# Performance work log

Measured on AMD Instinct MI355X. Metric: run time of the kernel, lower is better.

Reference implementation:

```python
import jax, jax.numpy as jnp
import numpy as np

C = 256
CK = C // 8  # key/query channels

def setup_inputs() -> dict:
    key = jax.random.key(0)
    ks = jax.random.split(key, 8)
    x = jax.random.normal(ks[0], (4, C, 64, 64), dtype=jnp.float32)
    # 1x1 conv weights stored as (out_ch, in_ch); bias (out_ch,)
    Wb = jax.random.normal(ks[1], (CK, C), dtype=jnp.float32) * (1.0 / np.sqrt(C))
    bb = jnp.zeros((CK,), dtype=jnp.float32)
    Wc = jax.random.normal(ks[2], (CK, C), dtype=jnp.float32) * (1.0 / np.sqrt(C))
    bc = jnp.zeros((CK,), dtype=jnp.float32)
    Wd = jax.random.normal(ks[3], (C, C), dtype=jnp.float32) * (1.0 / np.sqrt(C))
    bd = jnp.zeros((C,), dtype=jnp.float32)
    gamma = jnp.zeros((1,), dtype=jnp.float32)
    return {"x": x, "Wb": Wb, "bb": bb, "Wc": Wc, "bc": bc, "Wd": Wd, "bd": bd, "gamma": gamma}

def reference(x, Wb, bb, Wc, bc, Wd, bd, gamma):
    B, Cc, H, W = x.shape
    N = H * W
    xf = x.reshape(B, Cc, N)                                  # (B, C, N)
    # 1x1 convs == per-pixel linear projections
    b = jnp.einsum('kc,bcn->bnk', Wb, xf) + bb                # (B, N, CK) queries
    c = jnp.einsum('kc,bcn->bkn', Wc, xf) + bc[None, :, None] # (B, CK, N) keys
    d = jnp.einsum('oc,bcn->bon', Wd, xf) + bd[None, :, None] # (B, C, N) values
    attn = jax.nn.softmax(jnp.einsum('bnk,bkm->bnm', b, c), axis=-1)  # (B, N, N)
    out = jnp.einsum('bcm,bnm->bcn', d, attn).reshape(B, Cc, H, W)
    return gamma[0] * out + x
```

## Files before the change

### kernel.cpp

```cpp
#include <hip/hip_runtime.h>
#include <math.h>

#define B_  4
#define C_  256
#define N_  4096
#define NT  (N_ / 64)

typedef __attribute__((ext_vector_type(8)))  short v8s;
typedef __attribute__((ext_vector_type(4)))  float v4f;
typedef __attribute__((ext_vector_type(16))) float v16f;

__device__ inline unsigned short f2bf(float f) {
    unsigned u = __builtin_bit_cast(unsigned, f);
    unsigned r = (u + 0x7fffu + ((u >> 16) & 1u)) >> 16;
    return (unsigned short)r;
}
__device__ inline unsigned cvtpk(float lo, float hi) {
    unsigned r;
    asm("v_cvt_pk_bf16_f32 %0, %1, %2" : "=v"(r) : "v"(lo), "v"(hi));
    return r;
}
__device__ inline void swap32(unsigned &a, unsigned &b) {
    asm volatile("v_permlane32_swap_b32 %0, %1" : "+v"(a), "+v"(b));
}
__device__ inline void gl_lds16(const void* g, void* l) {
    __builtin_amdgcn_global_load_lds(
        (const __attribute__((address_space(1))) unsigned*)g,
        (__attribute__((address_space(3))) unsigned*)l, 16, 0, 0);
}

__global__ __launch_bounds__(256) void wcvt_kernel(
    const float* __restrict__ Wb, const float* __restrict__ Wc,
    const float* __restrict__ Wd, unsigned short* __restrict__ Wcat)
{
    int i = (blockIdx.x * 256 + threadIdx.x) * 4;
    int row = i >> 8, col = i & 255;
    const float* src;
    if (row < 256)      src = Wd + row * 256 + col;
    else if (row < 288) src = Wb + (row - 256) * 256 + col;
    else                src = Wc + (row - 288) * 256 + col;
    float4 v = *(const float4*)src;
    uint2 p;
    p.x = cvtpk(v.x, v.y);
    p.y = cvtpk(v.z, v.w);
    *(uint2*)(Wcat + i) = p;
}

#define PXS 264
__global__ __launch_bounds__(256, 2) void proj_mfma(
    const float* __restrict__ x, const unsigned short* __restrict__ Wcat,
    const float* __restrict__ bb, const float* __restrict__ bc,
    const float* __restrict__ bd,
    unsigned short* __restrict__ Q, unsigned short* __restrict__ K,
    unsigned short* __restrict__ V)
{
    __shared__ unsigned short Xs[32][PXS];
    const int t = threadIdx.x;
    const int w = t >> 6, l = t & 63, l16 = l & 15, lg = l >> 4;
    const int n0 = blockIdx.x * 32, b = blockIdx.y;

    {
        const int n = t & 31, g = t >> 5;
        const int c0 = g * 32;
        const float* xp = x + (size_t)b * C_ * N_ + n0 + n;
#pragma unroll
        for (int hf = 0; hf < 2; hf++) {
            unsigned pk[4];
#pragma unroll
            for (int j = 0; j < 4; j++) {
                int c = c0 + hf * 16 + 2 * j;
                pk[j] = cvtpk(xp[(size_t)c * N_], xp[(size_t)(c + 1) * N_]);
            }
            *(uint4*)&Xs[n][c0 + hf * 16] = make_uint4(pk[0], pk[1], pk[2], pk[3]);
        }
    }
    __syncthreads();

#pragma unroll 1
    for (int si = 0; si < 5; si++) {
        const int sub = w * 5 + si;

        v8s aw[8];
#pragma unroll
        for (int kk = 0; kk < 8; kk++)
            aw[kk] = *(const v8s*)(Wcat + (size_t)(sub * 16 + l16) * 256 + kk * 32 + lg * 8);

        v4f acc[2];
#pragma unroll
        for (int ns = 0; ns < 2; ns++) { v4f z = {0.f,0.f,0.f,0.f}; acc[ns] = z; }

#pragma unroll
        for (int kk = 0; kk < 8; kk++)
#pragma unroll
            for (int ns = 0; ns < 2; ns++) {
                v8s bx = *(const v8s*)&Xs[ns * 16 + l16][kk * 32 + lg * 8];
                acc[ns] = __builtin_amdgcn_mfma_f32_16x16x32_bf16(aw[kk], bx, acc[ns], 0, 0, 0);
            }

        if (sub < 16) {
            float bi[4];
#pragma unroll
            for (int r = 0; r < 4; r++) bi[r] = bd[sub * 16 + lg * 4 + r];
#pragma unroll
            for (int ns = 0; ns < 2; ns++) {
                const int n = n0 + ns * 16 + l16;
#pragma unroll
                for (int r = 0; r < 4; r++) {
                    int c = sub * 16 + lg * 4 + r;
                    V[((size_t)b * C_ + c) * N_ + n] = f2bf(acc[ns][r] + bi[r]);
                }
            }
        } else {
            const int qk = sub - 16;
            const bool isQ = (qk < 2);
            const int o0l = (qk & 1) * 16;
            const float* bias = isQ ? bb : bc;
            unsigned short* dst = isQ ? Q : K;
            float bi[4];
#pragma unroll
            for (int r = 0; r < 4; r++) bi[r] = bias[o0l + lg * 4 + r];
#pragma unroll
            for (int ns = 0; ns < 2; ns++) {
                const int n = n0 + ns * 16 + l16;
                uint2 pk;
                pk.x = cvtpk(acc[ns][0] + bi[0], acc[ns][1] + bi[1]);
                pk.y = cvtpk(acc[ns][2] + bi[2], acc[ns][3] + bi[3]);
                *(uint2*)(dst + ((size_t)b * N_ + n) * 32 + o0l + lg * 4) = pk;
            }
        }
    }
}

__global__ __launch_bounds__(256, 2) void attn_mfma(
    const unsigned short* __restrict__ Qg, const unsigned short* __restrict__ Kg,
    const unsigned short* __restrict__ Vg, const float* __restrict__ x,
    const float* __restrict__ gamma, float* __restrict__ out)
{
    __shared__ unsigned short Vs[2][64][64];

    const int t = threadIdx.x, l = t & 63, cl = l & 31, h = l >> 5;
    const int qs = t >> 6;
    const int i = blockIdx.x;
    const int xcd = i & 7, b = xcd >> 1, ch_hi = xcd & 1;
    const int rdec = i >> 3, ch = ch_hi * 2 + (rdec & 1), qb = rdec >> 1;
    const int q0 = qb * 128;
    const int q = q0 + qs * 32 + cl;

    const unsigned short* qp = Qg + ((size_t)b * N_ + q) * 32 + h * 8;
    const v8s bQ0 = *(const v8s*)(qp);
    const v8s bQ1 = *(const v8s*)(qp + 16);

    const unsigned short* kp = Kg + ((size_t)b * N_ + cl) * 32 + h * 8;
    const unsigned short* Vb = Vg + ((size_t)b * C_ + ch * 64) * N_;
    const int vrow = t >> 3;
    const int vslot = (t & 7) ^ (vrow & 7);
    const unsigned short* vsrc0 = Vb + (size_t)vrow * N_ + vslot * 8;
    const unsigned short* vsrc1 = Vb + (size_t)(32 + vrow) * N_ + vslot * 8;
    char* const ldsw = (char*)&Vs[0][0][0] + (t >> 6) * 1024;

    v16f acc0, acc1;
#pragma unroll
    for (int r = 0; r < 16; r++) { acc0[r] = 0.f; acc1[r] = 0.f; }
    float l_lane = 0.f;

    gl_lds16(vsrc0, ldsw);
    gl_lds16(vsrc1, ldsw + 4096);
    v8s kc0a = *(const v8s*)(kp);
    v8s kc0b = *(const v8s*)(kp + 16);
    v8s kc1a = *(const v8s*)(kp + 1024);
    v8s kc1b = *(const v8s*)(kp + 1024 + 16);
    __syncthreads();

    const int sx0 = ((0 * 2 + h) ^ (l & 7)) << 4;
    const int sx1 = ((1 * 2 + h) ^ (l & 7)) << 4;
    const int sx2 = ((2 * 2 + h) ^ (l & 7)) << 4;
    const int sx3 = ((3 * 2 + h) ^ (l & 7)) << 4;

#pragma unroll 1
    for (int it = 0; it < NT; it++) {
        const int buf = it & 1;
        v8s kn0a, kn0b, kn1a, kn1b;
        if (it + 1 < NT) {
            const int m1 = (it + 1) * 64;
            gl_lds16(vsrc0 + m1, ldsw + (buf ^ 1) * 8192);
            gl_lds16(vsrc1 + m1, ldsw + (buf ^ 1) * 8192 + 4096);
            const unsigned short* kpm = kp + (size_t)m1 * 32;
            kn0a = *(const v8s*)(kpm);
            kn0b = *(const v8s*)(kpm + 16);
            kn1a = *(const v8s*)(kpm + 1024);
            kn1b = *(const v8s*)(kpm + 1024 + 16);
        }

        v16f st0, st1;
#pragma unroll
        for (int r = 0; r < 16; r++) { st0[r] = 0.f; st1[r] = 0.f; }
        st0 = __builtin_amdgcn_mfma_f32_32x32x16_bf16(kc0a, bQ0, st0, 0, 0, 0);
        st0 = __builtin_amdgcn_mfma_f32_32x32x16_bf16(kc0b, bQ1, st0, 0, 0, 0);
        st1 = __builtin_amdgcn_mfma_f32_32x32x16_bf16(kc1a, bQ0, st1, 0, 0, 0);
        st1 = __builtin_amdgcn_mfma_f32_32x32x16_bf16(kc1b, bQ1, st1, 0, 0, 0);

        float ps = 0.f;
#pragma unroll
        for (int r = 0; r < 16; r++) { st0[r] = __expf(st0[r]); ps += st0[r]; }
#pragma unroll
        for (int r = 0; r < 16; r++) { st1[r] = __expf(st1[r]); ps += st1[r]; }
        l_lane += ps;

        unsigned pbw[4][4];
#pragma unroll
        for (int ms = 0; ms < 2; ms++) {
#pragma unroll
            for (int kl = 0; kl < 2; kl++) {
#pragma unroll
                for (int wl = 0; wl < 2; wl++) {
                    float e0, e1, f0, f1;
                    if (ms == 0) {
                        e0 = st0[(2*kl+0)*4 + 2*wl]; e1 = st0[(2*kl+0)*4 + 2*wl + 1];
                        f0 = st0[(2*kl+1)*4 + 2*wl]; f1 = st0[(2*kl+1)*4 + 2*wl + 1];
                    } else {
                        e0 = st1[(2*kl+0)*4 + 2*wl]; e1 = st1[(2*kl+0)*4 + 2*wl + 1];
                        f0 = st1[(2*kl+1)*4 + 2*wl]; f1 = st1[(2*kl+1)*4 + 2*wl + 1];
                    }
                    unsigned a = cvtpk(e0, e1);
                    unsigned c = cvtpk(f0, f1);
                    swap32(a, c);
                    pbw[ms * 2 + kl][wl]     = a;
                    pbw[ms * 2 + kl][2 + wl] = c;
                }
            }
        }

        const char* vbse = (const char*)&Vs[buf][0][0];
        {
            union { unsigned u[4]; v8s v; } pb;
#pragma unroll
            for (int ks2 = 0; ks2 < 4; ks2++) {
                pb.u[0] = pbw[ks2][0]; pb.u[1] = pbw[ks2][1];
                pb.u[2] = pbw[ks2][2]; pb.u[3] = pbw[ks2][3];
                const int sx = (ks2 == 0) ? sx0 : (ks2 == 1) ? sx1 : (ks2 == 2) ? sx2 : sx3;
                v8s a0 = *(const v8s*)(vbse + (cl << 7) + sx);
                v8s a1 = *(const v8s*)(vbse + ((32 + cl) << 7) + sx);
                acc0 = __builtin_amdgcn_mfma_f32_32x32x16_bf16(a0, pb.v, acc0, 0, 0, 0);
                acc1 = __builtin_amdgcn_mfma_f32_32x32x16_bf16(a1, pb.v, acc1, 0, 0, 0);
            }
        }

        __syncthreads();
        kc0a = kn0a; kc0b = kn0b; kc1a = kn1a; kc1b = kn1b;
    }

    float l_tot = l_lane + __shfl_xor(l_lane, 32);
    const float il = 1.0f / l_tot;
    const float gm = gamma[0];
#pragma unroll
    for (int cs = 0; cs < 2; cs++) {
#pragma unroll
        for (int r = 0; r < 16; r++) {
            int c = ch * 64 + cs * 32 + (r & 3) + 8 * (r >> 2) + 4 * h;
            size_t idx = ((size_t)b * C_ + c) * N_ + q;
            float a = (cs == 0) ? acc0[r] : acc1[r];
            out[idx] = gm * (a * il) + x[idx];
        }
    }
}

extern "C" void kernel_launch(void* const* d_in, const int* in_sizes, int n_in,
                              void* d_out, int out_size, void* d_ws, size_t ws_size,
                              hipStream_t stream)
{
    const float* x  = (const float*)d_in[0];
    const float* Wb = (const float*)d_in[1];
    const float* bb = (const float*)d_in[2];
    const float* Wc = (const float*)d_in[3];
    const float* bc = (const float*)d_in[4];
    const float* Wd = (const float*)d_in[5];
    const float* bd = (const float*)d_in[6];
    const float* gm = (const float*)d_in[7];
    float* out = (float*)d_out;

    unsigned short* Qw = (unsigned short*)d_ws;
    unsigned short* Kw = Qw + (size_t)B_ * N_ * 32;
    unsigned short* Vw = Kw + (size_t)B_ * N_ * 32;
    unsigned short* Wcat = Vw + (size_t)B_ * C_ * N_;

    wcvt_kernel<<<dim3(80), 256, 0, stream>>>(Wb, Wc, Wd, Wcat);
    proj_mfma<<<dim3(N_ / 32, B_), 256, 0, stream>>>(x, Wcat, bb, bc, bd, Qw, Kw, Vw);
    attn_mfma<<<dim3(512), 256, 0, stream>>>(Qw, Kw, Vw, x, gm, out);
}
```

Before: 163.8 us.

## Software-pipeline PV MFMA one tile behind QK, fold log2e into Q, vectorize x load

The attention loop now defers the P·V MFMAs for tile it-1 into iteration it, so they issue between the QK MFMAs and the exp of the current tile. This lets the matrix unit overlap with the softmax VALU work. The V LDS ring grows from 2 to 4 buffers so the deferred tile stays valid while later tiles load. Q is prescaled by log2(e) in the projection so the loop can use exp2f instead of __expf. The projection's x load is changed to float4 reads with scalar bf16 stores into LDS. Costs are more LDS per block, a larger live register set from the carried P fragments, and possible bank conflicts from the scalar LDS stores.

```diff
diff --git a/kernel.cpp b/kernel.cpp
--- a/kernel.cpp
+++ b/kernel.cpp
@@ -5,6 +5,7 @@
 #define C_  256
 #define N_  4096
 #define NT  (N_ / 64)
+#define LOG2E 1.44269504088896f
 
 typedef __attribute__((ext_vector_type(8)))  short v8s;
 typedef __attribute__((ext_vector_type(4)))  float v4f;
@@ -60,18 +61,16 @@
     const int n0 = blockIdx.x * 32, b = blockIdx.y;
 
     {
-        const int n = t & 31, g = t >> 5;
-        const int c0 = g * 32;
-        const float* xp = x + (size_t)b * C_ * N_ + n0 + n;
-#pragma unroll
-        for (int hf = 0; hf < 2; hf++) {
-            unsigned pk[4];
-#pragma unroll
-            for (int j = 0; j < 4; j++) {
-                int c = c0 + hf * 16 + 2 * j;
-                pk[j] = cvtpk(xp[(size_t)c * N_], xp[(size_t)(c + 1) * N_]);
-            }
-            *(uint4*)&Xs[n][c0 + hf * 16] = make_uint4(pk[0], pk[1], pk[2], pk[3]);
+        const int n4 = (t & 7) * 4, cb = t >> 3;
+        const float* xp = x + (size_t)b * C_ * N_ + n0 + n4;
+#pragma unroll
+        for (int r = 0; r < 8; r++) {
+            const int c = cb + r * 32;
+            float4 v = *(const float4*)(xp + (size_t)c * N_);
+            Xs[n4 + 0][c] = f2bf(v.x);
+            Xs[n4 + 1][c] = f2bf(v.y);
+            Xs[n4 + 2][c] = f2bf(v.z);
+            Xs[n4 + 3][c] = f2bf(v.w);
         }
     }
     __syncthreads();
@@ -79,7 +78,6 @@
 #pragma unroll 1
     for (int si = 0; si < 5; si++) {
         const int sub = w * 5 + si;
-
         v8s aw[8];
 #pragma unroll
         for (int kk = 0; kk < 8; kk++)
@@ -88,7 +86,6 @@
         v4f acc[2];
 #pragma unroll
         for (int ns = 0; ns < 2; ns++) { v4f z = {0.f,0.f,0.f,0.f}; acc[ns] = z; }
-
 #pragma unroll
         for (int kk = 0; kk < 8; kk++)
 #pragma unroll
@@ -116,6 +113,7 @@
             const int o0l = (qk & 1) * 16;
             const float* bias = isQ ? bb : bc;
             unsigned short* dst = isQ ? Q : K;
+            const float scl = isQ ? LOG2E : 1.0f;
             float bi[4];
 #pragma unroll
             for (int r = 0; r < 4; r++) bi[r] = bias[o0l + lg * 4 + r];
@@ -123,8 +121,8 @@
             for (int ns = 0; ns < 2; ns++) {
                 const int n = n0 + ns * 16 + l16;
                 uint2 pk;
-                pk.x = cvtpk(acc[ns][0] + bi[0], acc[ns][1] + bi[1]);
-                pk.y = cvtpk(acc[ns][2] + bi[2], acc[ns][3] + bi[3]);
+                pk.x = cvtpk((acc[ns][0] + bi[0]) * scl, (acc[ns][1] + bi[1]) * scl);
+                pk.y = cvtpk((acc[ns][2] + bi[2]) * scl, (acc[ns][3] + bi[3]) * scl);
                 *(uint2*)(dst + ((size_t)b * N_ + n) * 32 + o0l + lg * 4) = pk;
             }
         }
@@ -136,7 +134,7 @@
     const unsigned short* __restrict__ Vg, const float* __restrict__ x,
     const float* __restrict__ gamma, float* __restrict__ out)
 {
-    __shared__ unsigned short Vs[2][64][64];
+    __shared__ unsigned short Vs[4][64][64];
 
     const int t = threadIdx.x, l = t & 63, cl = l & 31, h = l >> 5;
     const int qs = t >> 6;
@@ -156,34 +154,36 @@
     const int vslot = (t & 7) ^ (vrow & 7);
     const unsigned short* vsrc0 = Vb + (size_t)vrow * N_ + vslot * 8;
     const unsigned short* vsrc1 = Vb + (size_t)(32 + vrow) * N_ + vslot * 8;
-    char* const ldsw = (char*)&Vs[0][0][0] + (t >> 6) * 1024;
+    const int wofs = (t >> 6) * 1024;
 
     v16f acc0, acc1;
 #pragma unroll
     for (int r = 0; r < 16; r++) { acc0[r] = 0.f; acc1[r] = 0.f; }
     float l_lane = 0.f;
 
-    gl_lds16(vsrc0, ldsw);
-    gl_lds16(vsrc1, ldsw + 4096);
+    gl_lds16(vsrc0, (char*)&Vs[0][0][0] + wofs);
+    gl_lds16(vsrc1, (char*)&Vs[0][0][0] + wofs + 4096);
     v8s kc0a = *(const v8s*)(kp);
     v8s kc0b = *(const v8s*)(kp + 16);
     v8s kc1a = *(const v8s*)(kp + 1024);
     v8s kc1b = *(const v8s*)(kp + 1024 + 16);
     __syncthreads();
 
-    const int sx0 = ((0 * 2 + h) ^ (l & 7)) << 4;
-    const int sx1 = ((1 * 2 + h) ^ (l & 7)) << 4;
-    const int sx2 = ((2 * 2 + h) ^ (l & 7)) << 4;
-    const int sx3 = ((3 * 2 + h) ^ (l & 7)) << 4;
+    const int sx0 = ((0 + h) ^ (l & 7)) << 4;
+    const int sx1 = ((2 + h) ^ (l & 7)) << 4;
+    const int sx2 = ((4 + h) ^ (l & 7)) << 4;
+    const int sx3 = ((6 + h) ^ (l & 7)) << 4;
+
+    v8s pbP0, pbP1, pbP2, pbP3;
 
 #pragma unroll 1
     for (int it = 0; it < NT; it++) {
-        const int buf = it & 1;
         v8s kn0a, kn0b, kn1a, kn1b;
         if (it + 1 < NT) {
             const int m1 = (it + 1) * 64;
-            gl_lds16(vsrc0 + m1, ldsw + (buf ^ 1) * 8192);
-            gl_lds16(vsrc1 + m1, ldsw + (buf ^ 1) * 8192 + 4096);
+            char* vd = (char*)&Vs[(it + 1) & 3][0][0] + wofs;
+            gl_lds16(vsrc0 + m1, vd);
+            gl_lds16(vsrc1 + m1, vd + 4096);
             const unsigned short* kpm = kp + (size_t)m1 * 32;
             kn0a = *(const v8s*)(kpm);
             kn0b = *(const v8s*)(kpm + 16);
@@ -199,11 +199,31 @@
         st1 = __builtin_amdgcn_mfma_f32_32x32x16_bf16(kc1a, bQ0, st1, 0, 0, 0);
         st1 = __builtin_amdgcn_mfma_f32_32x32x16_bf16(kc1b, bQ1, st1, 0, 0, 0);
 
+        if (it > 0) {
+            const char* vbse = (const char*)&Vs[(it - 1) & 3][0][0];
+            v8s a00 = *(const v8s*)(vbse + (cl << 7) + sx0);
+            v8s a10 = *(const v8s*)(vbse + ((32 + cl) << 7) + sx0);
+            v8s a01 = *(const v8s*)(vbse + (cl << 7) + sx1);
+            v8s a11 = *(const v8s*)(vbse + ((32 + cl) << 7) + sx1);
+            v8s a02 = *(const v8s*)(vbse + (cl << 7) + sx2);
+            v8s a12 = *(const v8s*)(vbse + ((32 + cl) << 7) + sx2);
+            v8s a03 = *(const v8s*)(vbse + (cl << 7) + sx3);
+            v8s a13 = *(const v8s*)(vbse + ((32 + cl) << 7) + sx3);
+            acc0 = __builtin_amdgcn_mfma_f32_32x32x16_bf16(a00, pbP0, acc0, 0, 0, 0);
+            acc1 = __builtin_amdgcn_mfma_f32_32x32x16_bf16(a10, pbP0, acc1, 0, 0, 0);
+            acc0 = __builtin_amdgcn_mfma_f32_32x32x16_bf16(a01, pbP1, acc0, 0, 0, 0);
+            acc1 = __builtin_amdgcn_mfma_f32_32x32x16_bf16(a11, pbP1, acc1, 0, 0, 0);
+            acc0 = __builtin_amdgcn_mfma_f32_32x32x16_bf16(a02, pbP2, acc0, 0, 0, 0);
+            acc1 = __builtin_amdgcn_mfma_f32_32x32x16_bf16(a12, pbP2, acc1, 0, 0, 0);
+            acc0 = __builtin_amdgcn_mfma_f32_32x32x16_bf16(a03, pbP3, acc0, 0, 0, 0);
+            acc1 = __builtin_amdgcn_mfma_f32_32x32x16_bf16(a13, pbP3, acc1, 0, 0, 0);
+        }
+
         float ps = 0.f;
 #pragma unroll
-        for (int r = 0; r < 16; r++) { st0[r] = __expf(st0[r]); ps += st0[r]; }
-#pragma unroll
-        for (int r = 0; r < 16; r++) { st1[r] = __expf(st1[r]); ps += st1[r]; }
+        for (int r = 0; r < 16; r++) { st0[r] = exp2f(st0[r]); ps += st0[r]; }
+#pragma unroll
+        for (int r = 0; r < 16; r++) { st1[r] = exp2f(st1[r]); ps += st1[r]; }
         l_lane += ps;
 
         unsigned pbw[4][4];
@@ -229,24 +249,36 @@
                 }
             }
         }
-
-        const char* vbse = (const char*)&Vs[buf][0][0];
         {
-            union { unsigned u[4]; v8s v; } pb;
-#pragma unroll
-            for (int ks2 = 0; ks2 < 4; ks2++) {
-                pb.u[0] = pbw[ks2][0]; pb.u[1] = pbw[ks2][1];
-                pb.u[2] = pbw[ks2][2]; pb.u[3] = pbw[ks2][3];
-                const int sx = (ks2 == 0) ? sx0 : (ks2 == 1) ? sx1 : (ks2 == 2) ? sx2 : sx3;
-                v8s a0 = *(const v8s*)(vbse + (cl << 7) + sx);
-                v8s a1 = *(const v8s*)(vbse + ((32 + cl) << 7) + sx);
-                acc0 = __builtin_amdgcn_mfma_f32_32x32x16_bf16(a0, pb.v, acc0, 0, 0, 0);
-                acc1 = __builtin_amdgcn_mfma_f32_32x32x16_bf16(a1, pb.v, acc1, 0, 0, 0);
-            }
+            union { unsigned u[4]; v8s v; } f;
+            f.u[0]=pbw[0][0]; f.u[1]=pbw[0][1]; f.u[2]=pbw[0][2]; f.u[3]=pbw[0][3]; pbP0=f.v;
+            f.u[0]=pbw[1][0]; f.u[1]=pbw[1][1]; f.u[2]=pbw[1][2]; f.u[3]=pbw[1][3]; pbP1=f.v;
+            f.u[0]=pbw[2][0]; f.u[1]=pbw[2][1]; f.u[2]=pbw[2][2]; f.u[3]=pbw[2][3]; pbP2=f.v;
+            f.u[0]=pbw[3][0]; f.u[1]=pbw[3][1]; f.u[2]=pbw[3][2]; f.u[3]=pbw[3][3]; pbP3=f.v;
         }
 
         __syncthreads();
         kc0a = kn0a; kc0b = kn0b; kc1a = kn1a; kc1b = kn1b;
+    }
+
+    {
+        const char* vbse = (const char*)&Vs[(NT - 1) & 3][0][0];
+        v8s a00 = *(const v8s*)(vbse + (cl << 7) + sx0);
+        v8s a10 = *(const v8s*)(vbse + ((32 + cl) << 7) + sx0);
+        v8s a01 = *(const v8s*)(vbse + (cl << 7) + sx1);
+        v8s a11 = *(const v8s*)(vbse + ((32 + cl) << 7) + sx1);
+        v8s a02 = *(const v8s*)(vbse + (cl << 7) + sx2);
+        v8s a12 = *(const v8s*)(vbse + ((32 + cl) << 7) + sx2);
+        v8s a03 = *(const v8s*)(vbse + (cl << 7) + sx3);
+        v8s a13 = *(const v8s*)(vbse + ((32 + cl) << 7) + sx3);
+        acc0 = __builtin_amdgcn_mfma_f32_32x32x16_bf16(a00, pbP0, acc0, 0, 0, 0);
+        acc1 = __builtin_amdgcn_mfma_f32_32x32x16_bf16(a10, pbP0, acc1, 0, 0, 0);
+        acc0 = __builtin_amdgcn_mfma_f32_32x32x16_bf16(a01, pbP1, acc0, 0, 0, 0);
+        acc1 = __builtin_amdgcn_mfma_f32_32x32x16_bf16(a11, pbP1, acc1, 0, 0, 0);
+        acc0 = __builtin_amdgcn_mfma_f32_32x32x16_bf16(a02, pbP2, acc0, 0, 0, 0);
+        acc1 = __builtin_amdgcn_mfma_f32_32x32x16_bf16(a12, pbP2, acc1, 0, 0, 0);
+        acc0 = __builtin_amdgcn_mfma_f32_32x32x16_bf16(a03, pbP3, acc0, 0, 0, 0);
+        acc1 = __builtin_amdgcn_mfma_f32_32x32x16_bf16(a13, pbP3, acc1, 0, 0, 0);
     }
 
     float l_tot = l_lane + __shfl_xor(l_lane, 32);
```

After: 193.4 us. 18.1% more time.
